# Performance work log

Hardware: AMD Instinct MI355X
Metric: run time of the kernel (lower is better)

## Reference

```python
import jax, jax.numpy as jnp
import numpy as np
from jax import lax

B, HP, WP, C, HEADS, SR = 8, 128, 128, 128, 2, 8
HEAD_DIM = C // HEADS
SCALE = HEAD_DIM ** -0.5
LN_EPS = 1e-5


def setup_inputs() -> dict:
    key = jax.random.key(0)
    ks = jax.random.split(key, 6)
    s = 0.02
    N = HP * WP
    return {
        "x": jax.random.normal(ks[0], (B, N, C), jnp.float32),
        "Hp": HP,
        "Wp": WP,
        "q_w": jax.random.normal(ks[1], (C, C), jnp.float32) * s,
        "q_b": jnp.zeros((C,), jnp.float32),
        "kv_w": jax.random.normal(ks[2], (2 * C, C), jnp.float32) * s,
        "kv_b": jnp.zeros((2 * C,), jnp.float32),
        "sr_w": jax.random.normal(ks[3], (C, C, SR, SR), jnp.float32) * s,  # OIHW
        "ln_g": jnp.ones((C,), jnp.float32),
        "ln_b": jnp.zeros((C,), jnp.float32),
        "proj_w": jax.random.normal(ks[4], (C, C), jnp.float32) * s,
        "proj_b": jnp.zeros((C,), jnp.float32),
    }


def reference(x, Hp, Wp, q_w, q_b, kv_w, kv_b, sr_w, ln_g, ln_b, proj_w, proj_b):
    Bn, N, Cd = x.shape
    # Q from full tokens: [B, H, N, hd]
    q = (x @ q_w.T + q_b).reshape(Bn, N, HEADS, HEAD_DIM).transpose(0, 2, 1, 3)
    # spatial reduction: conv kernel=stride=SR, no bias
    t2d = x.transpose(0, 2, 1).reshape(Bn, Cd, Hp, Wp)  # NCHW
    t2d = lax.conv_general_dilated(
        t2d, sr_w, window_strides=(SR, SR), padding="VALID",
        dimension_numbers=("NCHW", "OIHW", "NCHW"))
    Nk = t2d.shape[2] * t2d.shape[3]
    tok_kv = t2d.reshape(Bn, Cd, Nk).transpose(0, 2, 1)  # [B, Nk, C]
    # LayerNorm over channel dim
    mu = jnp.mean(tok_kv, axis=-1, keepdims=True)
    var = jnp.mean(jnp.square(tok_kv - mu), axis=-1, keepdims=True)
    tok_kv = (tok_kv - mu) * lax.rsqrt(var + LN_EPS) * ln_g + ln_b
    # K, V: [B, H, Nk, hd]
    kv = (tok_kv @ kv_w.T + kv_b).reshape(Bn, Nk, 2, HEADS, HEAD_DIM)
    kv = kv.transpose(2, 0, 3, 1, 4)
    k, v = kv[0], kv[1]
    # attention
    attn = jnp.einsum("bhnd,bhmd->bhnm", q, k) * SCALE
    attn = jax.nn.softmax(attn, axis=-1)
    out = jnp.einsum("bhnm,bhmd->bhnd", attn, v)
    out = out.transpose(0, 2, 1, 3).reshape(Bn, N, Cd)
    return out @ proj_w.T + proj_b
```

## Files before the change

kernel.cpp:

```cpp
#include <hip/hip_runtime.h>
#include <cstdint>

#define BB 8
#define NN 16384
#define CC 128
#define HEADS 2
#define HD 64
#define NK 256

#define OFF_CF   0
#define OFF_KVF  524288
#define OFF_QF   540672
#define OFF_PF   548864
#define OFF_K    557056
#define OFF_V    819200

typedef __attribute__((ext_vector_type(8))) __bf16 bf16x8;
typedef __attribute__((ext_vector_type(16))) float f32x16;
typedef __attribute__((ext_vector_type(4))) float f32x4;

union U4 { uint32_t u[4]; uint4 q; bf16x8 v; };

__device__ __forceinline__ uint32_t cvt_pk_bf16(float lo, float hi) {
  uint32_t r;
  asm("v_cvt_pk_bf16_f32 %0, %1, %2" : "=v"(r) : "v"(lo), "v"(hi));
  return r;
}
__device__ __forceinline__ void permswap(uint32_t& a, uint32_t& b) {
  asm("v_permlane32_swap_b32 %0, %1" : "+v"(a), "+v"(b));
}

__global__ __launch_bounds__(256) void prep_w(
    const float* __restrict__ sr_w, const float* __restrict__ proj_w,
    const float* __restrict__ kv_w, const float* __restrict__ q_w,
    float* __restrict__ ws) {
  int tid = blockIdx.x * 256 + threadIdx.x;
  if (tid < 524288) {
    int u = tid;
    int jp = u & 3, l = (u >> 2) & 63, nt = (u >> 8) & 7, ks = u >> 11;
    int k = ks * 32 + ((l >> 4) & 3) * 8 + jp * 2;
    int o = nt * 16 + (l & 15);
    int c = k & 127, p = k >> 7;
    ((uint32_t*)(ws + OFF_CF))[u] =
        cvt_pk_bf16(sr_w[o * 8192 + c * 64 + p], sr_w[o * 8192 + (c + 1) * 64 + p]);
  } else if (tid < 540672) {
    int u = tid - 524288;
    int jp = u & 3, l = (u >> 2) & 63, nt = (u >> 8) & 15, ks = u >> 12;
    int k = ks * 32 + ((l >> 4) & 3) * 8 + jp * 2;
    int o = nt * 16 + (l & 15);
    ((uint32_t*)(ws + OFF_KVF))[u] = cvt_pk_bf16(kv_w[o * 128 + k], kv_w[o * 128 + k + 1]);
  } else {
    int u = tid - 540672;
    const float* W = (u < 8192) ? q_w : proj_w;
    uint32_t* dst = (uint32_t*)(ws + ((u < 8192) ? OFF_QF : OFF_PF));
    u &= 8191;
    int jp = u & 3, l = (u >> 2) & 63, nt = (u >> 8) & 3, ks = u >> 10;
    int k = ks * 16 + (l >> 5) * 8 + jp * 2;
    int o = nt * 32 + (l & 31);
    dst[u] = cvt_pk_bf16(W[o * 128 + k], W[o * 128 + k + 1]);
  }
}

__global__ __launch_bounds__(512, 2) void conv_mfma(
    const float* __restrict__ x, const uint32_t* __restrict__ cf,
    const uint32_t* __restrict__ kvf, const float* __restrict__ kv_b,
    const float* __restrict__ ln_g, const float* __restrict__ ln_b,
    float* __restrict__ kbuf, float* __restrict__ vbuf) {
  extern __shared__ __align__(16) char lds[];
  const int t = threadIdx.x;
  const int l = t & 63, w = t >> 6;
  const int tg0 = blockIdx.x * 16;
  const int b   = tg0 >> 8;
  const int nk0 = tg0 & 255;
  const int ti  = nk0 >> 4;
  char* sreg = lds + w * 4096;
  const int col = l & 15, kg = (l >> 4) & 3;

  f32x4 acc[8];
  #pragma unroll
  for (int nt = 0; nt < 8; ++nt) acc[nt] = (f32x4)0.0f;

  for (int sub = 0; sub < 8; ++sub) {
    #pragma unroll
    for (int it = 0; it < 4; ++it) {
      int flat = it * 64 + l;
      int tk = flat >> 4, c16 = flat & 15;
      const float* src = x + ((size_t)b * NN + ((ti * 8 + w) * 128 + tk * 8 + sub)) * CC + c16 * 8;
      float4 a0 = *(const float4*)(src);
      float4 a1 = *(const float4*)(src + 4);
      U4 pk;
      pk.u[0] = cvt_pk_bf16(a0.x, a0.y); pk.u[1] = cvt_pk_bf16(a0.z, a0.w);
      pk.u[2] = cvt_pk_bf16(a1.x, a1.y); pk.u[3] = cvt_pk_bf16(a1.z, a1.w);
      *(uint4*)(sreg + tk * 256 + ((c16 * 16) ^ ((tk & 7) << 4))) = pk.q;
    }
    const int ksg0 = (w * 8 + sub) * 4;
    #pragma unroll
    for (int ksl = 0; ksl < 4; ++ksl) {
      U4 a;
      a.q = *(const uint4*)(sreg + col * 256 + ((ksl * 64 + kg * 16) ^ ((col & 7) << 4)));
      #pragma unroll
      for (int nt = 0; nt < 8; ++nt) {
        U4 bf_;
        bf_.q = *(const uint4*)(cf + (((ksg0 + ksl) * 8 + nt) * 64 + l) * 4);
        acc[nt] = __builtin_amdgcn_mfma_f32_16x16x32_bf16(a.v, bf_.v, acc[nt], 0, 0, 0);
      }
    }
  }

  float* rbuf = (float*)(lds + 32768);
  if (w >= 4) {
    float* dst = rbuf + (w - 4) * 2048;
    #pragma unroll
    for (int nt = 0; nt < 8; ++nt)
      #pragma unroll
      for (int r = 0; r < 4; ++r) dst[(kg * 4 + r) * 128 + nt * 16 + col] = acc[nt][r];
  }
  __syncthreads();
  if (w < 4) {
    const float* s1 = rbuf + w * 2048;
    #pragma unroll
    for (int nt = 0; nt < 8; ++nt)
      #pragma unroll
      for (int r = 0; r < 4; ++r) acc[nt][r] += s1[(kg * 4 + r) * 128 + nt * 16 + col];
    if (w >= 2) {
      float* dst = rbuf + w * 2048;
      #pragma unroll
      for (int nt = 0; nt < 8; ++nt)
        #pragma unroll
        for (int r = 0; r < 4; ++r) dst[(kg * 4 + r) * 128 + nt * 16 + col] = acc[nt][r];
    }
  }
  __syncthreads();
  if (w < 2) {
    const float* s2 = rbuf + (w + 2) * 2048;
    #pragma unroll
    for (int nt = 0; nt < 8; ++nt)
      #pragma unroll
      for (int r = 0; r < 4; ++r) acc[nt][r] += s2[(kg * 4 + r) * 128 + nt * 16 + col];
    if (w == 1) {
      float* dst = rbuf + 2048;
      #pragma unroll
      for (int nt = 0; nt < 8; ++nt)
        #pragma unroll
        for (int r = 0; r < 4; ++r) dst[(kg * 4 + r) * 128 + nt * 16 + col] = acc[nt][r];
    }
  }
  __syncthreads();
  if (w == 0) {
    const float* s3 = rbuf + 2048;
    #pragma unroll
    for (int nt = 0; nt < 8; ++nt)
      #pragma unroll
      for (int r = 0; r < 4; ++r) acc[nt][r] += s3[(kg * 4 + r) * 128 + nt * 16 + col];
    #pragma unroll
    for (int nt = 0; nt < 8; ++nt)
      #pragma unroll
      for (int r = 0; r < 4; ++r) rbuf[(kg * 4 + r) * 128 + nt * 16 + col] = acc[nt][r];
  }
  __syncthreads();

  char* abuf = lds + 65536;
  {
    const int tk = t >> 5, j = t & 31;
    float4 v4 = *(const float4*)(rbuf + tk * 128 + j * 4);
    float s  = v4.x + v4.y + v4.z + v4.w;
    float ss = v4.x * v4.x + v4.y * v4.y + v4.z * v4.z + v4.w * v4.w;
    #pragma unroll
    for (int m = 16; m; m >>= 1) { s += __shfl_xor(s, m); ss += __shfl_xor(ss, m); }
    float mu  = s * 0.0078125f;
    float var = fmaxf(ss * 0.0078125f - mu * mu, 0.f);
    float rs  = rsqrtf(var + 1e-5f);
    float4 g4 = *(const float4*)(ln_g + j * 4);
    float4 b4 = *(const float4*)(ln_b + j * 4);
    float y0 = (v4.x - mu) * rs * g4.x + b4.x;
    float y1 = (v4.y - mu) * rs * g4.y + b4.y;
    float y2 = (v4.z - mu) * rs * g4.z + b4.z;
    float y3 = (v4.w - mu) * rs * g4.w + b4.w;
    uint2 pk = make_uint2(cvt_pk_bf16(y0, y1), cvt_pk_bf16(y2, y3));
    *(uint2*)(abuf + tk * 256 + ((j * 8) ^ ((tk & 7) << 4))) = pk;
  }
  __syncthreads();

  f32x4 kacc[2];
  kacc[0] = (f32x4)0.0f; kacc[1] = (f32x4)0.0f;
  #pragma unroll
  for (int ks = 0; ks < 4; ++ks) {
    U4 a;
    a.q = *(const uint4*)(abuf + col * 256 + ((ks * 64 + kg * 16) ^ ((col & 7) << 4)));
    #pragma unroll
    for (int i = 0; i < 2; ++i) {
      int nt = w * 2 + i;
      U4 bf_;
      bf_.q = *(const uint4*)(kvf + ((ks * 16 + nt) * 64 + l) * 4);
      kacc[i] = __builtin_amdgcn_mfma_f32_16x16x32_bf16(a.v, bf_.v, kacc[i], 0, 0, 0);
    }
  }
  #pragma unroll
  for (int i = 0; i < 2; ++i) {
    int kvo = (w * 2 + i) * 16 + col;
    float bias = kv_b[kvo];
    float* obuf = (kvo >= 128) ? vbuf : kbuf;
    int h = (kvo >> 6) & 1, d = kvo & 63;
    #pragma unroll
    for (int r = 0; r < 4; ++r) {
      int tkr = kg * 4 + r;
      obuf[(((size_t)b * HEADS + h) * NK + nk0 + tkr) * HD + d] = kacc[i][r] + bias;
    }
  }
}

__global__ __launch_bounds__(256) void gemm128(
    const float* X, const uint32_t* __restrict__ frags,
    const float* __restrict__ bias, float scale, float* Y) {
  const int t = threadIdx.x;
  const int l = t & 63, wid = t >> 6;
  const int lq = l & 31, lh = l >> 5;
  const size_t rowbase = (size_t)blockIdx.x * 128 + wid * 32;
  const float* xrow = X + (rowbase + lq) * CC;

  f32x16 acc[4];
  #pragma unroll
  for (int nt = 0; nt < 4; ++nt) acc[nt] = (f32x16)0.0f;

  #pragma unroll
  for (int ks = 0; ks < 8; ++ks) {
    float4 a0 = *(const float4*)(xrow + ks * 16 + lh * 8);
    float4 a1 = *(const float4*)(xrow + ks * 16 + lh * 8 + 4);
    U4 af;
    af.u[0] = cvt_pk_bf16(a0.x, a0.y); af.u[1] = cvt_pk_bf16(a0.z, a0.w);
    af.u[2] = cvt_pk_bf16(a1.x, a1.y); af.u[3] = cvt_pk_bf16(a1.z, a1.w);
    #pragma unroll
    for (int nt = 0; nt < 4; ++nt) {
      U4 bf_;
      bf_.q = *(const uint4*)(frags + ((ks * 4 + nt) * 64 + l) * 4);
      acc[nt] = __builtin_amdgcn_mfma_f32_32x32x16_bf16(af.v, bf_.v, acc[nt], 0, 0, 0);
    }
  }
  #pragma unroll
  for (int nt = 0; nt < 4; ++nt) {
    int o = nt * 32 + lq;
    float bv = bias[o];
    #pragma unroll
    for (int r = 0; r < 16; ++r) {
      int m = (r & 3) + 8 * (r >> 2) + 4 * lh;
      Y[(rowbase + m) * CC + o] = (acc[nt][r] + bv) * scale;
    }
  }
}

__global__ __launch_bounds__(256, 2) void attn_mfma(
    const float* __restrict__ qsrc, const float* __restrict__ kbuf,
    const float* __restrict__ vbuf, float* __restrict__ out) {
  __shared__ __align__(16) char lds[65536];
  const int t  = threadIdx.x;
  const int l  = t & 63, wid = t >> 6;
  const int lq = l & 31, lh = l >> 5;
  const int bh = blockIdx.x >> 7;
  const int b  = bh >> 1, h = bh & 1;
  const int qbase = (blockIdx.x & 127) * 128;

  U4 qb[4];
  {
    const float* q0 = qsrc + ((size_t)b * NN + qbase + wid * 32 + lq) * CC + h * 64;
    #pragma unroll
    for (int kg = 0; kg < 4; ++kg) {
      float4 x0 = *(const float4*)(q0 + kg * 16 + lh * 8);
      float4 x1 = *(const float4*)(q0 + kg * 16 + lh * 8 + 4);
      qb[kg].u[0] = cvt_pk_bf16(x0.x, x0.y); qb[kg].u[1] = cvt_pk_bf16(x0.z, x0.w);
      qb[kg].u[2] = cvt_pk_bf16(x1.x, x1.y); qb[kg].u[3] = cvt_pk_bf16(x1.z, x1.w);
    }
  }

  {
    const float* kb = kbuf + (size_t)bh * NK * HD;
    #pragma unroll
    for (int it = 0; it < 16; ++it) {
      int flat = it * 256 + t;
      int key = flat >> 4, j = flat & 15;
      float4 kv = *(const float4*)(kb + key * HD + j * 4);
      int byte = (key * 128 + j * 8) ^ ((key & 7) << 4);
      *(uint2*)(lds + byte) = make_uint2(cvt_pk_bf16(kv.x, kv.y), cvt_pk_bf16(kv.z, kv.w));
    }
    const float* vb = vbuf + (size_t)bh * NK * HD;
    int d = t & 63, kb4 = t >> 6;
    #pragma unroll
    for (int k0 = 0; k0 < 64; k0 += 4) {
      int k = kb4 * 64 + k0;
      float v0 = vb[(k + 0) * HD + d], v1 = vb[(k + 1) * HD + d];
      float v2 = vb[(k + 2) * HD + d], v3 = vb[(k + 3) * HD + d];
      int byte = 32768 + ((d * 512 + k * 2) ^ ((d & 7) << 4));
      *(uint2*)(lds + byte) = make_uint2(cvt_pk_bf16(v0, v1), cvt_pk_bf16(v2, v3));
    }
  }
  __syncthreads();

  f32x16 p[8];
  #pragma unroll
  for (int kt = 0; kt < 8; ++kt) p[kt] = (f32x16)0.0f;
  #pragma unroll
  for (int kt = 0; kt < 8; ++kt) {
    const int key = kt * 32 + lq;
    #pragma unroll
    for (int kg = 0; kg < 4; ++kg) {
      U4 a;
      int byte = (key * 128 + kg * 32 + lh * 16) ^ ((key & 7) << 4);
      a.q = *(const uint4*)(lds + byte);
      p[kt] = __builtin_amdgcn_mfma_f32_32x32x16_bf16(a.v, qb[kg].v, p[kt], 0, 0, 0);
    }
  }

  float mx = -1e30f;
  #pragma unroll
  for (int kt = 0; kt < 8; ++kt)
    #pragma unroll
    for (int i = 0; i < 16; ++i) mx = fmaxf(mx, p[kt][i]);
  mx = fmaxf(mx, __shfl_xor(mx, 32));
  float sum = 0.f;
  #pragma unroll
  for (int kt = 0; kt < 8; ++kt)
    #pragma unroll
    for (int i = 0; i < 16; ++i) { float e = __expf(p[kt][i] - mx); p[kt][i] = e; sum += e; }
  sum += __shfl_xor(sum, 32);
  const float inv = 1.f / sum;
  #pragma unroll
  for (int kt = 0; kt < 8; ++kt)
    #pragma unroll
    for (int i = 0; i < 16; ++i) p[kt][i] *= inv;

  f32x16 oacc0 = (f32x16)0.0f, oacc1 = (f32x16)0.0f;
  #pragma unroll
  for (int kt = 0; kt < 8; ++kt) {
    uint32_t x0 = cvt_pk_bf16(p[kt][0],  p[kt][1]);
    uint32_t x1 = cvt_pk_bf16(p[kt][2],  p[kt][3]);
    uint32_t y0 = cvt_pk_bf16(p[kt][4],  p[kt][5]);
    uint32_t y1 = cvt_pk_bf16(p[kt][6],  p[kt][7]);
    permswap(x0, y0); permswap(x1, y1);
    U4 pa0; pa0.u[0] = x0; pa0.u[1] = x1; pa0.u[2] = y0; pa0.u[3] = y1;
    uint32_t x2 = cvt_pk_bf16(p[kt][8],  p[kt][9]);
    uint32_t x3 = cvt_pk_bf16(p[kt][10], p[kt][11]);
    uint32_t y2 = cvt_pk_bf16(p[kt][12], p[kt][13]);
    uint32_t y3 = cvt_pk_bf16(p[kt][14], p[kt][15]);
    permswap(x2, y2); permswap(x3, y3);
    U4 pa1; pa1.u[0] = x2; pa1.u[1] = x3; pa1.u[2] = y2; pa1.u[3] = y3;
    #pragma unroll
    for (int dt = 0; dt < 2; ++dt) {
      int d = dt * 32 + lq;
      U4 vb0, vb1;
      int byte0 = 32768 + ((d * 512 + kt * 64 + lh * 16) ^ ((d & 7) << 4));
      int byte1 = 32768 + ((d * 512 + kt * 64 + 32 + lh * 16) ^ ((d & 7) << 4));
      vb0.q = *(const uint4*)(lds + byte0);
      vb1.q = *(const uint4*)(lds + byte1);
      f32x16& oa = dt ? oacc1 : oacc0;
      oa = __builtin_amdgcn_mfma_f32_32x32x16_bf16(pa0.v, vb0.v, oa, 0, 0, 0);
      oa = __builtin_amdgcn_mfma_f32_32x32x16_bf16(pa1.v, vb1.v, oa, 0, 0, 0);
    }
  }

  float* ob = out + ((size_t)b * NN + qbase + wid * 32) * CC + h * 64;
  #pragma unroll
  for (int reg = 0; reg < 16; ++reg) {
    int q = (reg & 3) + 8 * (reg >> 2) + 4 * lh;
    ob[q * CC + lq]      = oacc0[reg];
    ob[q * CC + 32 + lq] = oacc1[reg];
  }
}

extern "C" void kernel_launch(void* const* d_in, const int* in_sizes, int n_in,
                              void* d_out, int out_size, void* d_ws, size_t ws_size,
                              hipStream_t stream) {
  const float* x      = (const float*)d_in[0];
  const float* q_w    = (const float*)d_in[3];
  const float* q_b    = (const float*)d_in[4];
  const float* kv_w   = (const float*)d_in[5];
  const float* kv_b   = (const float*)d_in[6];
  const float* sr_w   = (const float*)d_in[7];
  const float* ln_g   = (const float*)d_in[8];
  const float* ln_b   = (const float*)d_in[9];
  const float* proj_w = (const float*)d_in[10];
  const float* proj_b = (const float*)d_in[11];
  float* out = (float*)d_out;
  float* ws  = (float*)d_ws;

  hipLaunchKernelGGL(prep_w, dim3(2176), dim3(256), 0, stream, sr_w, proj_w, kv_w, q_w, ws);
  hipLaunchKernelGGL(conv_mfma, dim3(128), dim3(512), 69632, stream,
                     x, (const uint32_t*)(ws + OFF_CF), (const uint32_t*)(ws + OFF_KVF),
                     kv_b, ln_g, ln_b, ws + OFF_K, ws + OFF_V);
  hipLaunchKernelGGL(gemm128, dim3(1024), dim3(256), 0, stream,
                     x, (const uint32_t*)(ws + OFF_QF), q_b, 0.125f, out);
  hipLaunchKernelGGL(attn_mfma, dim3(2048), dim3(256), 0, stream,
                     out, ws + OFF_K, ws + OFF_V, out);
  hipLaunchKernelGGL(gemm128, dim3(1024), dim3(256), 0, stream,
                     out, (const uint32_t*)(ws + OFF_PF), proj_b, 1.0f, out);
}
```

Baseline: 134.3 us.

## Split conv reduction across blocks with partial sums and separate LN/KV kernel

The strided conv kernel previously ran on only 128 blocks, each reducing all 8 kernel rows. It now splits that reduction across up to 4 blocks per output tile, each writing a partial sum to workspace. A new kernel then adds the partials and applies LayerNorm and the KV projection. This fills more of the GPU's compute units, at the cost of an extra launch and a round trip of partials through global memory; the split factor depends on the workspace size.

```diff
diff --git a/kernel.cpp b/kernel.cpp
--- a/kernel.cpp
+++ b/kernel.cpp
@@ -14,6 +14,7 @@
 #define OFF_PF   548864
 #define OFF_K    557056
 #define OFF_V    819200
+#define OFF_PART 1081344
 
 typedef __attribute__((ext_vector_type(8))) __bf16 bf16x8;
 typedef __attribute__((ext_vector_type(16))) float f32x16;
@@ -49,30 +50,33 @@
     int k = ks * 32 + ((l >> 4) & 3) * 8 + jp * 2;
     int o = nt * 16 + (l & 15);
     ((uint32_t*)(ws + OFF_KVF))[u] = cvt_pk_bf16(kv_w[o * 128 + k], kv_w[o * 128 + k + 1]);
-  } else {
+  } else if (tid < 548864) {
     int u = tid - 540672;
-    const float* W = (u < 8192) ? q_w : proj_w;
-    uint32_t* dst = (uint32_t*)(ws + ((u < 8192) ? OFF_QF : OFF_PF));
-    u &= 8191;
     int jp = u & 3, l = (u >> 2) & 63, nt = (u >> 8) & 3, ks = u >> 10;
     int k = ks * 16 + (l >> 5) * 8 + jp * 2;
     int o = nt * 32 + (l & 31);
-    dst[u] = cvt_pk_bf16(W[o * 128 + k], W[o * 128 + k + 1]);
-  }
-}
-
-__global__ __launch_bounds__(512, 2) void conv_mfma(
+    ((uint32_t*)(ws + OFF_QF))[u] = cvt_pk_bf16(q_w[o * 128 + k], q_w[o * 128 + k + 1]);
+  } else {
+    int u = tid - 548864;
+    int jp = u & 3, l = (u >> 2) & 63, nt = (u >> 8) & 3, ks = u >> 10;
+    int k = ks * 16 + (l >> 5) * 8 + jp * 2;
+    int o = nt * 32 + (l & 31);
+    ((uint32_t*)(ws + OFF_PF))[u] = cvt_pk_bf16(proj_w[o * 128 + k], proj_w[o * 128 + k + 1]);
+  }
+}
+
+template<int NSUB>
+__global__ __launch_bounds__(512, 2) void conv_partial(
     const float* __restrict__ x, const uint32_t* __restrict__ cf,
-    const uint32_t* __restrict__ kvf, const float* __restrict__ kv_b,
-    const float* __restrict__ ln_g, const float* __restrict__ ln_b,
-    float* __restrict__ kbuf, float* __restrict__ vbuf) {
+    float* __restrict__ partial) {
   extern __shared__ __align__(16) char lds[];
   const int t = threadIdx.x;
   const int l = t & 63, w = t >> 6;
-  const int tg0 = blockIdx.x * 16;
-  const int b   = tg0 >> 8;
-  const int nk0 = tg0 & 255;
-  const int ti  = nk0 >> 4;
+  const int NQ = 8 / NSUB;
+  const int tile = blockIdx.x / NQ;
+  const int khq  = blockIdx.x % NQ;
+  const int b  = tile >> 4;
+  const int ti = tile & 15;
   char* sreg = lds + w * 4096;
   const int col = l & 15, kg = (l >> 4) & 3;
 
@@ -80,7 +84,9 @@
   #pragma unroll
   for (int nt = 0; nt < 8; ++nt) acc[nt] = (f32x4)0.0f;
 
-  for (int sub = 0; sub < 8; ++sub) {
+  #pragma unroll
+  for (int si = 0; si < NSUB; ++si) {
+    const int sub = khq * NSUB + si;
     #pragma unroll
     for (int it = 0; it < 4; ++it) {
       int flat = it * 64 + l;
@@ -151,20 +157,36 @@
     #pragma unroll
     for (int nt = 0; nt < 8; ++nt)
       #pragma unroll
-      for (int r = 0; r < 4; ++r) acc[nt][r] += s3[(kg * 4 + r) * 128 + nt * 16 + col];
-    #pragma unroll
-    for (int nt = 0; nt < 8; ++nt)
-      #pragma unroll
-      for (int r = 0; r < 4; ++r) rbuf[(kg * 4 + r) * 128 + nt * 16 + col] = acc[nt][r];
-  }
-  __syncthreads();
-
-  char* abuf = lds + 65536;
+      for (int r = 0; r < 4; ++r) {
+        acc[nt][r] += s3[(kg * 4 + r) * 128 + nt * 16 + col];
+        rbuf[(kg * 4 + r) * 128 + nt * 16 + col] = acc[nt][r];
+      }
+  }
+  __syncthreads();
+  float4 vv = ((const float4*)rbuf)[t];
+  ((float4*)(partial + ((size_t)khq * 128 + tile) * 2048))[t] = vv;
+}
+
+__global__ __launch_bounds__(512) void reduce_ln_kv(
+    const float* __restrict__ partial, int nq,
+    const uint32_t* __restrict__ kvf, const float* __restrict__ kv_b,
+    const float* __restrict__ ln_g, const float* __restrict__ ln_b,
+    float* __restrict__ kbuf, float* __restrict__ vbuf) {
+  __shared__ __align__(16) char abuf[4096];
+  const int t = threadIdx.x;
+  const int l = t & 63, w = t >> 6;
+  const int tile = blockIdx.x;
+  const int b = tile >> 4, nk0 = (tile & 15) * 16;
+
+  float4 a = make_float4(0.f, 0.f, 0.f, 0.f);
+  for (int i = 0; i < nq; ++i) {
+    float4 p = *(const float4*)(partial + ((size_t)i * 128 + tile) * 2048 + t * 4);
+    a.x += p.x; a.y += p.y; a.z += p.z; a.w += p.w;
+  }
   {
     const int tk = t >> 5, j = t & 31;
-    float4 v4 = *(const float4*)(rbuf + tk * 128 + j * 4);
-    float s  = v4.x + v4.y + v4.z + v4.w;
-    float ss = v4.x * v4.x + v4.y * v4.y + v4.z * v4.z + v4.w * v4.w;
+    float s  = a.x + a.y + a.z + a.w;
+    float ss = a.x * a.x + a.y * a.y + a.z * a.z + a.w * a.w;
     #pragma unroll
     for (int m = 16; m; m >>= 1) { s += __shfl_xor(s, m); ss += __shfl_xor(ss, m); }
     float mu  = s * 0.0078125f;
@@ -172,27 +194,28 @@
     float rs  = rsqrtf(var + 1e-5f);
     float4 g4 = *(const float4*)(ln_g + j * 4);
     float4 b4 = *(const float4*)(ln_b + j * 4);
-    float y0 = (v4.x - mu) * rs * g4.x + b4.x;
-    float y1 = (v4.y - mu) * rs * g4.y + b4.y;
-    float y2 = (v4.z - mu) * rs * g4.z + b4.z;
-    float y3 = (v4.w - mu) * rs * g4.w + b4.w;
-    uint2 pk = make_uint2(cvt_pk_bf16(y0, y1), cvt_pk_bf16(y2, y3));
-    *(uint2*)(abuf + tk * 256 + ((j * 8) ^ ((tk & 7) << 4))) = pk;
-  }
-  __syncthreads();
-
+    float y0 = (a.x - mu) * rs * g4.x + b4.x;
+    float y1 = (a.y - mu) * rs * g4.y + b4.y;
+    float y2 = (a.z - mu) * rs * g4.z + b4.z;
+    float y3 = (a.w - mu) * rs * g4.w + b4.w;
+    *(uint2*)(abuf + tk * 256 + ((j * 8) ^ ((tk & 7) << 4))) =
+        make_uint2(cvt_pk_bf16(y0, y1), cvt_pk_bf16(y2, y3));
+  }
+  __syncthreads();
+
+  const int col = l & 15, kg = (l >> 4) & 3;
   f32x4 kacc[2];
   kacc[0] = (f32x4)0.0f; kacc[1] = (f32x4)0.0f;
   #pragma unroll
   for (int ks = 0; ks < 4; ++ks) {
-    U4 a;
-    a.q = *(const uint4*)(abuf + col * 256 + ((ks * 64 + kg * 16) ^ ((col & 7) << 4)));
+    U4 aa;
+    aa.q = *(const uint4*)(abuf + col * 256 + ((ks * 64 + kg * 16) ^ ((col & 7) << 4)));
     #pragma unroll
     for (int i = 0; i < 2; ++i) {
       int nt = w * 2 + i;
       U4 bf_;
       bf_.q = *(const uint4*)(kvf + ((ks * 16 + nt) * 64 + l) * 4);
-      kacc[i] = __builtin_amdgcn_mfma_f32_16x16x32_bf16(a.v, bf_.v, kacc[i], 0, 0, 0);
+      kacc[i] = __builtin_amdgcn_mfma_f32_16x16x32_bf16(aa.v, bf_.v, kacc[i], 0, 0, 0);
     }
   }
   #pragma unroll
@@ -381,14 +404,28 @@
   float* out = (float*)d_out;
   float* ws  = (float*)d_ws;
 
-  hipLaunchKernelGGL(prep_w, dim3(2176), dim3(256), 0, stream, sr_w, proj_w, kv_w, q_w, ws);
-  hipLaunchKernelGGL(conv_mfma, dim3(128), dim3(512), 69632, stream,
-                     x, (const uint32_t*)(ws + OFF_CF), (const uint32_t*)(ws + OFF_KVF),
-                     kv_b, ln_g, ln_b, ws + OFF_K, ws + OFF_V);
-  hipLaunchKernelGGL(gemm128, dim3(1024), dim3(256), 0, stream,
-                     x, (const uint32_t*)(ws + OFF_QF), q_b, 0.125f, out);
-  hipLaunchKernelGGL(attn_mfma, dim3(2048), dim3(256), 0, stream,
-                     out, ws + OFF_K, ws + OFF_V, out);
-  hipLaunchKernelGGL(gemm128, dim3(1024), dim3(256), 0, stream,
-                     out, (const uint32_t*)(ws + OFF_PF), proj_b, 1.0f, out);
-}
+  prep_w<<<dim3(2176), dim3(256), 0, stream>>>(sr_w, proj_w, kv_w, q_w, ws);
+
+  int nq = 1;
+  if (ws_size >= (size_t)(OFF_PART + 4 * 262144) * 4) nq = 4;
+  else if (ws_size >= (size_t)(OFF_PART + 2 * 262144) * 4) nq = 2;
+
+  const uint32_t* cf = (const uint32_t*)(ws + OFF_CF);
+  float* part = ws + OFF_PART;
+  if (nq == 4)
+    conv_partial<2><<<dim3(512), dim3(512), 65536, stream>>>(x, cf, part);
+  else if (nq == 2)
+    conv_partial<4><<<dim3(256), dim3(512), 65536, stream>>>(x, cf, part);
+  else
+    conv_partial<8><<<dim3(128), dim3(512), 65536, stream>>>(x, cf, part);
+
+  reduce_ln_kv<<<dim3(128), dim3(512), 0, stream>>>(
+      part, nq, (const uint32_t*)(ws + OFF_KVF), kv_b, ln_g, ln_b,
+      ws + OFF_K, ws + OFF_V);
+  gemm128<<<dim3(1024), dim3(256), 0, stream>>>(
+      x, (const uint32_t*)(ws + OFF_QF), q_b, 0.125f, out);
+  attn_mfma<<<dim3(2048), dim3(256), 0, stream>>>(
+      out, ws + OFF_K, ws + OFF_V, out);
+  gemm128<<<dim3(1024), dim3(256), 0, stream>>>(
+      out, (const uint32_t*)(ws + OFF_PF), proj_b, 1.0f, out);
+}
```

Result: faster. 121.0 us (-9.9%).
